# Kernel tuning notes

Hardware: AMD Instinct MI355X
Metric: run time of the kernel (lower is better)

The kernel has to match this reference:

```python
import jax, jax.numpy as jnp
import numpy as np

B, N_PER, E_PER = 100, 1000, 12000  # graphs, nodes/graph, edges/graph
N, E = B * N_PER, B * E_PER
K = int(np.ceil(0.8 * N_PER))  # TopKPooling ratio=0.8 -> 800 kept nodes/graph


def setup_inputs() -> dict:
    key = jax.random.key(0)
    ks = jax.random.split(key, 16)
    g = jnp.repeat(jnp.arange(B, dtype=jnp.int64), E_PER)
    src = g * N_PER + jax.random.randint(ks[0], (E,), 0, N_PER)
    dst = g * N_PER + jax.random.randint(ks[1], (E,), 0, N_PER)
    edge_index = jnp.stack([src, dst]).astype(jnp.int64)
    edge_attr = jax.random.uniform(ks[2], (E,), dtype=jnp.float32) + 0.1  # positive edge weights
    x = jax.random.normal(ks[3], (N, 3), dtype=jnp.float32)
    batch = jnp.repeat(jnp.arange(B, dtype=jnp.int64), N_PER)
    s = 0.1
    return {
        'x': x, 'edge_index': edge_index, 'edge_attr': edge_attr, 'batch': batch,
        'conv1_w': jax.random.normal(ks[4], (3, 64), dtype=jnp.float32) * s,
        'conv1_b': jnp.zeros((64,), dtype=jnp.float32),
        'conv2_w': jax.random.normal(ks[5], (64, 64), dtype=jnp.float32) * s,
        'conv2_b': jnp.zeros((64,), dtype=jnp.float32),
        'pool_w': jax.random.normal(ks[6], (64,), dtype=jnp.float32) * s,
        'lin1_w': jax.random.normal(ks[7], (64, 64), dtype=jnp.float32) * s,
        'lin1_b': jnp.zeros((64,), dtype=jnp.float32),
        'lin2_w': jax.random.normal(ks[8], (64, 32), dtype=jnp.float32) * s,
        'lin2_b': jnp.zeros((32,), dtype=jnp.float32),
        'lin3_w': jax.random.normal(ks[9], (32, 1), dtype=jnp.float32) * s,
        'lin3_b': jnp.zeros((1,), dtype=jnp.float32),
    }


def gcn_conv(x, row, col, ew, W, b):
    # PyG GCNConv with edge_weight and implicit self-loops (weight 1):
    # deg[i] = sum_{e: col=i} ew[e] + 1;  norm_e = d^{-1/2}[row]*ew*d^{-1/2}[col]
    h = x @ W  # [N, out]
    deg = jax.ops.segment_sum(ew, col, num_segments=N) + 1.0
    dinv = jax.lax.rsqrt(deg)
    msg = (dinv[row] * ew * dinv[col])[:, None] * h[row]  # [E, out]
    out = jax.ops.segment_sum(msg, col, num_segments=N)
    out = out + (dinv * dinv)[:, None] * h  # self-loop term
    return out + b


def reference(x, edge_index, edge_attr, batch, conv1_w, conv1_b, conv2_w, conv2_b,
              pool_w, lin1_w, lin1_b, lin2_w, lin2_b, lin3_w, lin3_b):
    row, col = edge_index[0], edge_index[1]
    h = jax.nn.relu(gcn_conv(x, row, col, edge_attr, conv1_w, conv1_b))
    x1 = h.reshape(B, N_PER, 64).mean(axis=1)  # global_mean_pool (equal-size graphs)
    h = jax.nn.relu(gcn_conv(h, row, col, edge_attr, conv2_w, conv2_b))
    # TopKPooling: score = tanh(x.w / ||w||), keep top-K per graph, gate by score
    score = jnp.tanh(h @ pool_w / jnp.linalg.norm(pool_w))  # [N]
    score_bn = score.reshape(B, N_PER)
    vals, idx = jax.lax.top_k(score_bn, K)  # [B, K]
    h_bn = h.reshape(B, N_PER, 64)
    h_sel = jnp.take_along_axis(h_bn, idx[..., None], axis=1) * vals[..., None]
    x2 = h_sel.mean(axis=1)  # global_mean_pool on pooled graph
    z = x1 + x2
    z = jax.nn.relu(z @ lin1_w + lin1_b)
    z = jax.nn.relu(z @ lin2_w + lin2_b)  # dropout is identity in eval mode
    out = jax.nn.sigmoid(z @ lin3_w + lin3_b)[:, 0]
    return out
```

## Files before the change

kernel.cpp:

```cpp
#include <hip/hip_runtime.h>

#define B_G   100
#define N_PER 1000
#define E_PER 12000
#define NTOT  (B_G * N_PER)
#define ETOT  (B_G * E_PER)
#define KSEL  800
#define EPT   12

typedef __attribute__((ext_vector_type(8))) short short8;
typedef __attribute__((ext_vector_type(4))) float float4_;

__device__ __forceinline__ unsigned short f2bf(float f) {
    unsigned u = __float_as_uint(f);
    u += 0x7fffu + ((u >> 16) & 1u);
    return (unsigned short)(u >> 16);
}
__device__ __forceinline__ float bf2f(unsigned short h) {
    return __uint_as_float(((unsigned)h) << 16);
}

__device__ __forceinline__ void load_row_frag(
    const unsigned char* h1s, int src, int kgrp, short8& r0, short8& r1) {
    unsigned a0 = (unsigned)src * 128u + (((unsigned)(kgrp ^ (src & 7))) << 4);
    r0 = *(const short8*)(h1s + a0);
    r1 = *(const short8*)(h1s + (a0 ^ 64u));
}

__global__ __launch_bounds__(1024) void k_all(
    const int* __restrict__ ei, const float* __restrict__ ew,
    const float* __restrict__ x,
    const float* __restrict__ w1, const float* __restrict__ b1,
    const float* __restrict__ w2, const float* __restrict__ b2,
    const float* __restrict__ pw,
    const float* __restrict__ l1w, const float* __restrict__ l1b,
    const float* __restrict__ l2w, const float* __restrict__ l2b,
    const float* __restrict__ l3w, const float* __restrict__ l3b,
    unsigned* __restrict__ csr, float* __restrict__ out) {
    __shared__ __align__(16) unsigned char smem[152832];
    unsigned char* h1s = smem;
    unsigned short* h1u = (unsigned short*)smem;
    int*   ends = (int*)(smem + 128000);
    float* dl   = (float*)(smem + 132096);
    float* x1b  = (float*)(smem + 136192);
    unsigned char* uA = smem + 136448;

    int b = blockIdx.x, tid = threadIdx.x;
    int wid = tid >> 6, lane = tid & 63;
    int gbase = b * N_PER, ebase = b * E_PER;

    int esrc[EPT], edst[EPT]; float eww[EPT];
    int ne = (tid < (E_PER - (EPT - 1) * 1024)) ? EPT : EPT - 1;
#pragma unroll
    for (int i = 0; i < EPT; i++) {
        if (i < ne) {
            int e = tid + i * 1024;
            esrc[i] = ei[ebase + e] - gbase;
            edst[i] = ei[ETOT + ebase + e] - gbase;
            eww[i]  = ew[ebase + e];
        }
    }
    float* wsum = (float*)uA;
    int*   posc = (int*)(uA + 4096);
    ends[tid] = 0;
    wsum[tid] = 0.f;
    __syncthreads();
#pragma unroll
    for (int i = 0; i < EPT; i++)
        if (i < ne) {
            atomicAdd(&ends[edst[i]], 1);
            atomicAdd(&wsum[edst[i]], eww[i]);
        }
    __syncthreads();
    int v = ends[tid];
    int sc = v;
#pragma unroll
    for (int m = 1; m < 64; m <<= 1) {
        int t = __shfl_up(sc, m);
        if (lane >= m) sc += t;
    }
    int* wpart = (int*)x1b;
    if (lane == 63) wpart[wid] = sc;
    __syncthreads();
    if (tid < 16) {
        int s2 = wpart[tid];
#pragma unroll
        for (int m = 1; m < 16; m <<= 1) {
            int t = __shfl_up(s2, m);
            if (tid >= m) s2 += t;
        }
        wpart[tid] = s2;
    }
    __syncthreads();
    int incl = sc + (wid > 0 ? wpart[wid - 1] : 0);
    ends[tid] = incl;
    posc[tid] = incl - v;
    dl[tid] = rsqrtf(wsum[tid] + 1.0f);
    __syncthreads();
#pragma unroll
    for (int i = 0; i < EPT; i++)
        if (i < ne) {
            float cf = dl[esrc[i]] * eww[i] * dl[edst[i]];
            int p = atomicAdd(&posc[edst[i]], 1);
            csr[ebase + p] = ((unsigned)f2bf(cf) << 16) | (unsigned)esrc[i];
        }
    __syncthreads();
    float* aggv = (float*)uA;
    if (tid < N_PER) {
        int s = (tid > 0) ? ends[tid - 1] : 0;
        int e = ends[tid];
        float a0 = 0.f, a1 = 0.f, a2 = 0.f;
        for (int k = s; k < e; k++) {
            unsigned q = csr[ebase + k];
            float cf = __uint_as_float(q & 0xFFFF0000u);
            const float* xs = x + (size_t)(gbase + (int)(q & 0xFFFFu)) * 3;
            a0 += cf * xs[0]; a1 += cf * xs[1]; a2 += cf * xs[2];
        }
        float d2 = dl[tid] * dl[tid];
        const float* xn = x + (size_t)(gbase + tid) * 3;
        aggv[tid * 3 + 0] = a0 + d2 * xn[0];
        aggv[tid * 3 + 1] = a1 + d2 * xn[1];
        aggv[tid * 3 + 2] = a2 + d2 * xn[2];
    }
    __syncthreads();
    {
        float w0 = w1[lane], w1v = w1[64 + lane], w2v = w1[128 + lane], bf = b1[lane];
        float* sred = (float*)(uA + 12288);
        float px = 0.f;
        int swoff = (lane & 7);
        for (int node = wid; node < N_PER; node += 16) {
            float a0 = aggv[node * 3], a1 = aggv[node * 3 + 1], a2 = aggv[node * 3 + 2];
            float h = fmaxf(a0 * w0 + a1 * w1v + a2 * w2v + bf, 0.f);
            h1u[node * 64 + ((((lane >> 3) ^ (node & 7))) << 3) + swoff] = f2bf(h);
            px += h;
        }
        sred[wid * 64 + lane] = px;
        __syncthreads();
        if (tid < 64) {
            float t = 0.f;
            for (int r = 0; r < 16; r++) t += sred[r * 64 + tid];
            x1b[tid] = t * (1.0f / N_PER);
        }
    }
    __syncthreads();
    int kgrp = lane >> 4, nloc = lane & 15;
    short8 AfS[4][2];
#pragma unroll
    for (int ti = 0; ti < 4; ti++) {
        int t = wid + ti * 16;
        if (t >= 63) continue;
        int li = t * 16 + nloc;
        bool valid = li < N_PER;
        float acc[16];
        if (valid) {
            float d2 = dl[li] * dl[li];
            short8 r0, r1;
            load_row_frag(h1s, li, kgrp, r0, r1);
#pragma unroll
            for (int j = 0; j < 8; j++) {
                acc[j]     = d2 * bf2f((unsigned short)r0[j]);
                acc[8 + j] = d2 * bf2f((unsigned short)r1[j]);
            }
        } else {
#pragma unroll
            for (int j = 0; j < 16; j++) acc[j] = 0.f;
        }
        int s = 0, cnt = 0;
        if (valid) {
            s = (li > 0) ? ends[li - 1] : 0;
            cnt = ends[li] - s;
        }
        int mx = cnt;
#pragma unroll
        for (int m = 1; m < 16; m <<= 1) mx = max(mx, __shfl_xor(mx, m));
        int base = ebase + s;
        int cl = max(cnt - 1, 0);
        unsigned q = csr[min(base, ETOT - 1)];
        for (int k = 0; k < mx; k++) {
            unsigned qn = csr[min(base + min(k + 1, cl), ETOT - 1)];
            if (k < cnt) {
                int src = (int)(q & 0xFFFFu);
                float cf = __uint_as_float(q & 0xFFFF0000u);
                short8 r0, r1;
                load_row_frag(h1s, src, kgrp, r0, r1);
#pragma unroll
                for (int j = 0; j < 8; j++) {
                    acc[j]     += cf * bf2f((unsigned short)r0[j]);
                    acc[8 + j] += cf * bf2f((unsigned short)r1[j]);
                }
            }
            q = qn;
        }
        short8 a0, a1;
#pragma unroll
        for (int j = 0; j < 8; j++) {
            a0[j] = (short)f2bf(acc[j]);
            a1[j] = (short)f2bf(acc[8 + j]);
        }
        AfS[ti][0] = a0;
        AfS[ti][1] = a1;
    }
    __syncthreads();
    unsigned long long* keys = (unsigned long long*)uA;
    {
        short8 Bf[2][4];
#pragma unroll
        for (int kh = 0; kh < 2; ++kh)
#pragma unroll
            for (int c = 0; c < 4; ++c) {
                short8 t;
#pragma unroll
                for (int j = 0; j < 8; ++j)
                    t[j] = (short)f2bf(w2[(kh * 32 + kgrp * 8 + j) * 64 + c * 16 + nloc]);
                Bf[kh][c] = t;
            }
        float b2c[4], pwc[4];
#pragma unroll
        for (int c = 0; c < 4; ++c) {
            b2c[c] = b2[c * 16 + nloc];
            pwc[c] = pw[c * 16 + nloc];
        }
        float invn;
        {
            float p = pw[lane], pn = p * p;
#pragma unroll
            for (int m = 32; m; m >>= 1) pn += __shfl_xor(pn, m);
            invn = rsqrtf(pn);
        }
        if (tid >= N_PER) keys[tid] = 0ull;
#pragma unroll
        for (int ti = 0; ti < 4; ti++) {
            int t = wid + ti * 16;
            if (t >= 63) continue;
            float4_ accv[4];
#pragma unroll
            for (int c = 0; c < 4; ++c) accv[c] = (float4_){0.f, 0.f, 0.f, 0.f};
#pragma unroll
            for (int kh = 0; kh < 2; ++kh)
#pragma unroll
                for (int c = 0; c < 4; ++c)
                    accv[c] = __builtin_amdgcn_mfma_f32_16x16x32_bf16(AfS[ti][kh], Bf[kh][c], accv[c], 0, 0, 0);
#pragma unroll
            for (int r2 = 0; r2 < 4; ++r2) {
                int li2 = t * 16 + kgrp * 4 + r2;
                bool valid2 = li2 < N_PER;
                float sp = 0.f;
#pragma unroll
                for (int c = 0; c < 4; ++c) {
                    float hv = fmaxf(accv[c][r2] + b2c[c], 0.f);
                    sp += hv * pwc[c];
                    if (valid2) {
                        int f = c * 16 + nloc;
                        h1u[li2 * 64 + ((((f >> 3) ^ (li2 & 7))) << 3) + (f & 7)] = f2bf(hv);
                    }
                }
#pragma unroll
                for (int m = 1; m < 16; m <<= 1) sp += __shfl_xor(sp, m);
                if (valid2 && nloc == 0) {
                    float scv = tanhf(sp * invn);
                    unsigned bits = __float_as_uint(scv);
                    unsigned u = (bits & 0x80000000u) ? ~bits : (bits | 0x80000000u);
                    keys[li2] = ((unsigned long long)u << 32) | (unsigned)(1023 - li2);
                }
            }
        }
    }
    __syncthreads();
    {
        unsigned long long key = keys[tid];
        for (int k = 2; k <= 1024; k <<= 1) {
            for (int j = k >> 1; j > 0; j >>= 1) {
                bool desc = (tid & k) == 0;
                unsigned long long p;
                if (j >= 64) {
                    keys[tid] = key;
                    __syncthreads();
                    p = keys[tid ^ j];
                    __syncthreads();
                } else {
                    p = __shfl_xor(key, j);
                }
                bool low = (tid & j) == 0;
                bool sw = low ? (desc ? (key < p) : (key > p))
                              : (desc ? (p < key) : (p > key));
                if (sw) key = p;
            }
        }
        keys[tid] = key;
    }
    __syncthreads();
    float* red   = (float*)(uA + 8192);
    float* a1buf = (float*)(uA + 12288);
    float* a2buf = (float*)(uA + 12544);
    float* zbuf  = (float*)(uA + 12672);
    {
        int f = tid & 63, w16 = tid >> 6;
        float acc = 0.f;
        for (int r = w16; r < KSEL; r += 16) {
            unsigned long long key = keys[r];
            int idx = 1023 - (int)(key & 0xFFFFFFFFu);
            unsigned u = (unsigned)(key >> 32);
            unsigned bits = (u & 0x80000000u) ? (u & 0x7FFFFFFFu) : ~u;
            float val = __uint_as_float(bits);
            acc += val * bf2f(h1u[idx * 64 + ((((f >> 3) ^ (idx & 7))) << 3) + (f & 7)]);
        }
        red[tid] = acc;
    }
    __syncthreads();
    if (tid < 64) {
        float s2 = 0.f;
        for (int ww = 0; ww < 16; ww++) s2 += red[ww * 64 + tid];
        zbuf[tid] = x1b[tid] + s2 * (1.0f / KSEL);
    }
    __syncthreads();
    if (tid < 64) {
        float a = l1b[tid];
        for (int k = 0; k < 64; k++) a += zbuf[k] * l1w[k * 64 + tid];
        a1buf[tid] = fmaxf(a, 0.f);
    }
    __syncthreads();
    if (tid < 32) {
        float a = l2b[tid];
        for (int k = 0; k < 64; k++) a += a1buf[k] * l2w[k * 32 + tid];
        a2buf[tid] = fmaxf(a, 0.f);
    }
    __syncthreads();
    if (tid == 0) {
        float t = l3b[0];
        for (int k = 0; k < 32; k++) t += a2buf[k] * l3w[k];
        out[b] = 1.0f / (1.0f + expf(-t));
    }
}

extern "C" void kernel_launch(void* const* d_in, const int* in_sizes, int n_in,
                              void* d_out, int out_size, void* d_ws, size_t ws_size,
                              hipStream_t stream) {
    const float* x   = (const float*)d_in[0];
    const int*   ei  = (const int*)d_in[1];
    const float* ew  = (const float*)d_in[2];
    const float* c1w = (const float*)d_in[4];
    const float* c1b = (const float*)d_in[5];
    const float* c2w = (const float*)d_in[6];
    const float* c2b = (const float*)d_in[7];
    const float* pw  = (const float*)d_in[8];
    const float* l1w = (const float*)d_in[9];
    const float* l1b = (const float*)d_in[10];
    const float* l2w = (const float*)d_in[11];
    const float* l2b = (const float*)d_in[12];
    const float* l3w = (const float*)d_in[13];
    const float* l3b = (const float*)d_in[14];
    float* out = (float*)d_out;
    unsigned* csr = (unsigned*)d_ws;
    (void)ws_size; (void)in_sizes; (void)n_in; (void)out_size;

    k_all<<<B_G, 1024, 0, stream>>>(ei, ew, x, c1w, c1b, c2w, c2b, pw,
                                    l1w, l1b, l2w, l2b, l3w, l3b, csr, out);
}
```

Measured before the change: 191.9 us.

## Split each graph across two blocks and move top-k pooling into second kernel

The fused per-graph kernel becomes two blocks per graph. Each block recomputes degrees and the full layer-1 features but builds CSR and runs the layer-2 MFMA only for its half of the destination nodes. It writes h2, scores and the layer-1 mean to global workspace, and a second kernel does the top-k sort, gated pooling and MLP. Layer-1 aggregation now uses shared-memory atomics on a staged copy of x instead of a CSR gather from global memory. The aim is to fill more of the GPU's compute units (100 blocks to 200). The cost is duplicated per-graph preprocessing, an extra launch, and a global round-trip for h2.

```diff
diff --git a/kernel.cpp b/kernel.cpp
--- a/kernel.cpp
+++ b/kernel.cpp
@@ -7,6 +7,8 @@
 #define ETOT  (B_G * E_PER)
 #define KSEL  800
 #define EPT   12
+#define HALF  512
+#define CSR_CAP 8192
 
 typedef __attribute__((ext_vector_type(8))) short short8;
 typedef __attribute__((ext_vector_type(4))) float float4_;
@@ -27,27 +29,32 @@
     r1 = *(const short8*)(h1s + (a0 ^ 64u));
 }
 
-__global__ __launch_bounds__(1024) void k_all(
+__global__ __launch_bounds__(1024) void k_main(
     const int* __restrict__ ei, const float* __restrict__ ew,
     const float* __restrict__ x,
     const float* __restrict__ w1, const float* __restrict__ b1,
     const float* __restrict__ w2, const float* __restrict__ b2,
     const float* __restrict__ pw,
-    const float* __restrict__ l1w, const float* __restrict__ l1b,
-    const float* __restrict__ l2w, const float* __restrict__ l2b,
-    const float* __restrict__ l3w, const float* __restrict__ l3b,
-    unsigned* __restrict__ csr, float* __restrict__ out) {
-    __shared__ __align__(16) unsigned char smem[152832];
+    unsigned* __restrict__ csr, unsigned short* __restrict__ h2g,
+    float* __restrict__ scoreg, float* __restrict__ x1g) {
+    __shared__ __align__(16) unsigned char smem[160768];
     unsigned char* h1s = smem;
     unsigned short* h1u = (unsigned short*)smem;
     int*   ends = (int*)(smem + 128000);
     float* dl   = (float*)(smem + 132096);
-    float* x1b  = (float*)(smem + 136192);
-    unsigned char* uA = smem + 136448;
-
-    int b = blockIdx.x, tid = threadIdx.x;
-    int wid = tid >> 6, lane = tid & 63;
-    int gbase = b * N_PER, ebase = b * E_PER;
+    float* xl   = (float*)(smem + 136192);
+    float* sred = (float*)(smem + 136192);
+    unsigned char* U = smem + 148480;
+    int*   posc  = (int*)U;
+    float* wsum  = (float*)(U + 4096);
+    int*   wpart = (int*)(U + 8192);
+    float* aggv  = (float*)U;
+
+    int blk = blockIdx.x;
+    int g = blk >> 1, h = blk & 1;
+    int tid = threadIdx.x, wid = tid >> 6, lane = tid & 63;
+    int gbase = g * N_PER, ebase = g * E_PER;
+    unsigned* csrg = csr + (size_t)blk * CSR_CAP;
 
     int esrc[EPT], edst[EPT]; float eww[EPT];
     int ne = (tid < (E_PER - (EPT - 1) * 1024)) ? EPT : EPT - 1;
@@ -60,16 +67,15 @@
             eww[i]  = ew[ebase + e];
         }
     }
-    float* wsum = (float*)uA;
-    int*   posc = (int*)(uA + 4096);
     ends[tid] = 0;
     wsum[tid] = 0.f;
+    for (int i = tid; i < N_PER * 3; i += 1024) xl[i] = x[(size_t)gbase * 3 + i];
     __syncthreads();
 #pragma unroll
     for (int i = 0; i < EPT; i++)
         if (i < ne) {
-            atomicAdd(&ends[edst[i]], 1);
             atomicAdd(&wsum[edst[i]], eww[i]);
+            if ((edst[i] >> 9) == h) atomicAdd(&ends[edst[i]], 1);
         }
     __syncthreads();
     int v = ends[tid];
@@ -79,7 +85,6 @@
         int t = __shfl_up(sc, m);
         if (lane >= m) sc += t;
     }
-    int* wpart = (int*)x1b;
     if (lane == 63) wpart[wid] = sc;
     __syncthreads();
     if (tid < 16) {
@@ -99,57 +104,51 @@
     __syncthreads();
 #pragma unroll
     for (int i = 0; i < EPT; i++)
+        if (i < ne && (edst[i] >> 9) == h) {
+            float cf = dl[esrc[i]] * eww[i] * dl[edst[i]];
+            int p = atomicAdd(&posc[edst[i]], 1);
+            csrg[p] = ((unsigned)f2bf(cf) << 16) | (unsigned)esrc[i];
+        }
+    __syncthreads();
+    for (int i = tid; i < N_PER; i += 1024) {
+        float d2 = dl[i] * dl[i];
+        aggv[i * 3 + 0] = d2 * xl[i * 3 + 0];
+        aggv[i * 3 + 1] = d2 * xl[i * 3 + 1];
+        aggv[i * 3 + 2] = d2 * xl[i * 3 + 2];
+    }
+    __syncthreads();
+#pragma unroll
+    for (int i = 0; i < EPT; i++)
         if (i < ne) {
             float cf = dl[esrc[i]] * eww[i] * dl[edst[i]];
-            int p = atomicAdd(&posc[edst[i]], 1);
-            csr[ebase + p] = ((unsigned)f2bf(cf) << 16) | (unsigned)esrc[i];
-        }
-    __syncthreads();
-    float* aggv = (float*)uA;
-    if (tid < N_PER) {
-        int s = (tid > 0) ? ends[tid - 1] : 0;
-        int e = ends[tid];
-        float a0 = 0.f, a1 = 0.f, a2 = 0.f;
-        for (int k = s; k < e; k++) {
-            unsigned q = csr[ebase + k];
-            float cf = __uint_as_float(q & 0xFFFF0000u);
-            const float* xs = x + (size_t)(gbase + (int)(q & 0xFFFFu)) * 3;
-            a0 += cf * xs[0]; a1 += cf * xs[1]; a2 += cf * xs[2];
-        }
-        float d2 = dl[tid] * dl[tid];
-        const float* xn = x + (size_t)(gbase + tid) * 3;
-        aggv[tid * 3 + 0] = a0 + d2 * xn[0];
-        aggv[tid * 3 + 1] = a1 + d2 * xn[1];
-        aggv[tid * 3 + 2] = a2 + d2 * xn[2];
-    }
+            atomicAdd(&aggv[edst[i] * 3 + 0], cf * xl[esrc[i] * 3 + 0]);
+            atomicAdd(&aggv[edst[i] * 3 + 1], cf * xl[esrc[i] * 3 + 1]);
+            atomicAdd(&aggv[edst[i] * 3 + 2], cf * xl[esrc[i] * 3 + 2]);
+        }
     __syncthreads();
     {
         float w0 = w1[lane], w1v = w1[64 + lane], w2v = w1[128 + lane], bf = b1[lane];
-        float* sred = (float*)(uA + 12288);
         float px = 0.f;
-        int swoff = (lane & 7);
         for (int node = wid; node < N_PER; node += 16) {
             float a0 = aggv[node * 3], a1 = aggv[node * 3 + 1], a2 = aggv[node * 3 + 2];
-            float h = fmaxf(a0 * w0 + a1 * w1v + a2 * w2v + bf, 0.f);
-            h1u[node * 64 + ((((lane >> 3) ^ (node & 7))) << 3) + swoff] = f2bf(h);
-            px += h;
+            float hv = fmaxf(a0 * w0 + a1 * w1v + a2 * w2v + bf, 0.f);
+            h1u[node * 64 + ((((lane >> 3) ^ (node & 7))) << 3) + (lane & 7)] = f2bf(hv);
+            px += hv;
         }
         sred[wid * 64 + lane] = px;
-        __syncthreads();
-        if (tid < 64) {
-            float t = 0.f;
-            for (int r = 0; r < 16; r++) t += sred[r * 64 + tid];
-            x1b[tid] = t * (1.0f / N_PER);
-        }
-    }
-    __syncthreads();
+    }
+    __syncthreads();
+    if (h == 0 && tid < 64) {
+        float t = 0.f;
+        for (int r = 0; r < 16; r++) t += sred[r * 64 + tid];
+        x1g[g * 64 + tid] = t * (1.0f / N_PER);
+    }
     int kgrp = lane >> 4, nloc = lane & 15;
-    short8 AfS[4][2];
-#pragma unroll
-    for (int ti = 0; ti < 4; ti++) {
+    short8 AfS[2][2];
+#pragma unroll
+    for (int ti = 0; ti < 2; ti++) {
         int t = wid + ti * 16;
-        if (t >= 63) continue;
-        int li = t * 16 + nloc;
+        int li = h * HALF + t * 16 + nloc;
         bool valid = li < N_PER;
         float acc[16];
         if (valid) {
@@ -173,11 +172,10 @@
         int mx = cnt;
 #pragma unroll
         for (int m = 1; m < 16; m <<= 1) mx = max(mx, __shfl_xor(mx, m));
-        int base = ebase + s;
         int cl = max(cnt - 1, 0);
-        unsigned q = csr[min(base, ETOT - 1)];
+        unsigned q = csrg[min(s, CSR_CAP - 1)];
         for (int k = 0; k < mx; k++) {
-            unsigned qn = csr[min(base + min(k + 1, cl), ETOT - 1)];
+            unsigned qn = csrg[min(s + min(k + 1, cl), CSR_CAP - 1)];
             if (k < cnt) {
                 int src = (int)(q & 0xFFFFu);
                 float cf = __uint_as_float(q & 0xFFFF0000u);
@@ -200,8 +198,6 @@
         AfS[ti][0] = a0;
         AfS[ti][1] = a1;
     }
-    __syncthreads();
-    unsigned long long* keys = (unsigned long long*)uA;
     {
         short8 Bf[2][4];
 #pragma unroll
@@ -227,11 +223,9 @@
             for (int m = 32; m; m >>= 1) pn += __shfl_xor(pn, m);
             invn = rsqrtf(pn);
         }
-        if (tid >= N_PER) keys[tid] = 0ull;
-#pragma unroll
-        for (int ti = 0; ti < 4; ti++) {
+#pragma unroll
+        for (int ti = 0; ti < 2; ti++) {
             int t = wid + ti * 16;
-            if (t >= 63) continue;
             float4_ accv[4];
 #pragma unroll
             for (int c = 0; c < 4; ++c) accv[c] = (float4_){0.f, 0.f, 0.f, 0.f};
@@ -242,28 +236,41 @@
                     accv[c] = __builtin_amdgcn_mfma_f32_16x16x32_bf16(AfS[ti][kh], Bf[kh][c], accv[c], 0, 0, 0);
 #pragma unroll
             for (int r2 = 0; r2 < 4; ++r2) {
-                int li2 = t * 16 + kgrp * 4 + r2;
+                int li2 = h * HALF + t * 16 + kgrp * 4 + r2;
                 bool valid2 = li2 < N_PER;
                 float sp = 0.f;
 #pragma unroll
                 for (int c = 0; c < 4; ++c) {
                     float hv = fmaxf(accv[c][r2] + b2c[c], 0.f);
                     sp += hv * pwc[c];
-                    if (valid2) {
-                        int f = c * 16 + nloc;
-                        h1u[li2 * 64 + ((((f >> 3) ^ (li2 & 7))) << 3) + (f & 7)] = f2bf(hv);
-                    }
+                    if (valid2) h2g[(size_t)(gbase + li2) * 64 + c * 16 + nloc] = f2bf(hv);
                 }
 #pragma unroll
                 for (int m = 1; m < 16; m <<= 1) sp += __shfl_xor(sp, m);
-                if (valid2 && nloc == 0) {
-                    float scv = tanhf(sp * invn);
-                    unsigned bits = __float_as_uint(scv);
-                    unsigned u = (bits & 0x80000000u) ? ~bits : (bits | 0x80000000u);
-                    keys[li2] = ((unsigned long long)u << 32) | (unsigned)(1023 - li2);
-                }
-            }
-        }
+                if (valid2 && nloc == 0) scoreg[gbase + li2] = tanhf(sp * invn);
+            }
+        }
+    }
+}
+
+__global__ __launch_bounds__(1024) void k_post(
+    const float* __restrict__ scoreg, const unsigned short* __restrict__ h2g,
+    const float* __restrict__ x1g,
+    const float* __restrict__ l1w, const float* __restrict__ l1b,
+    const float* __restrict__ l2w, const float* __restrict__ l2b,
+    const float* __restrict__ l3w, const float* __restrict__ l3b,
+    float* __restrict__ out) {
+    __shared__ unsigned long long keys[1024];
+    __shared__ float red[1024];
+    __shared__ float zbuf[64], a1buf[64], a2buf[32];
+    int b = blockIdx.x, tid = threadIdx.x;
+    if (tid < N_PER) {
+        float sc = scoreg[b * N_PER + tid];
+        unsigned bits = __float_as_uint(sc);
+        unsigned u = (bits & 0x80000000u) ? ~bits : (bits | 0x80000000u);
+        keys[tid] = ((unsigned long long)u << 32) | (unsigned)(1023 - tid);
+    } else {
+        keys[tid] = 0ull;
     }
     __syncthreads();
     {
@@ -289,10 +296,6 @@
         keys[tid] = key;
     }
     __syncthreads();
-    float* red   = (float*)(uA + 8192);
-    float* a1buf = (float*)(uA + 12288);
-    float* a2buf = (float*)(uA + 12544);
-    float* zbuf  = (float*)(uA + 12672);
     {
         int f = tid & 63, w16 = tid >> 6;
         float acc = 0.f;
@@ -302,7 +305,7 @@
             unsigned u = (unsigned)(key >> 32);
             unsigned bits = (u & 0x80000000u) ? (u & 0x7FFFFFFFu) : ~u;
             float val = __uint_as_float(bits);
-            acc += val * bf2f(h1u[idx * 64 + ((((f >> 3) ^ (idx & 7))) << 3) + (f & 7)]);
+            acc += val * bf2f(h2g[(size_t)(b * N_PER + idx) * 64 + f]);
         }
         red[tid] = acc;
     }
@@ -310,7 +313,7 @@
     if (tid < 64) {
         float s2 = 0.f;
         for (int ww = 0; ww < 16; ww++) s2 += red[ww * 64 + tid];
-        zbuf[tid] = x1b[tid] + s2 * (1.0f / KSEL);
+        zbuf[tid] = x1g[b * 64 + tid] + s2 * (1.0f / KSEL);
     }
     __syncthreads();
     if (tid < 64) {
@@ -350,9 +353,18 @@
     const float* l3w = (const float*)d_in[13];
     const float* l3b = (const float*)d_in[14];
     float* out = (float*)d_out;
-    unsigned* csr = (unsigned*)d_ws;
+
+    char* ws = (char*)d_ws;
+    size_t o = 0;
+    auto alloc = [&](size_t bytes) { size_t cur = o; o += (bytes + 511) & ~(size_t)511; return cur; };
+    unsigned*       csr    = (unsigned*)(ws + alloc((size_t)B_G * 2 * CSR_CAP * 4));
+    unsigned short* h2g    = (unsigned short*)(ws + alloc((size_t)NTOT * 64 * 2));
+    float*          scoreg = (float*)(ws + alloc((size_t)NTOT * 4));
+    float*          x1g    = (float*)(ws + alloc((size_t)B_G * 64 * 4));
     (void)ws_size; (void)in_sizes; (void)n_in; (void)out_size;
 
-    k_all<<<B_G, 1024, 0, stream>>>(ei, ew, x, c1w, c1b, c2w, c2b, pw,
-                                    l1w, l1b, l2w, l2b, l3w, l3b, csr, out);
-}
+    k_main<<<B_G * 2, 1024, 0, stream>>>(ei, ew, x, c1w, c1b, c2w, c2b, pw,
+                                         csr, h2g, scoreg, x1g);
+    k_post<<<B_G, 1024, 0, stream>>>(scoreg, h2g, x1g,
+                                     l1w, l1b, l2w, l2b, l3w, l3b, out);
+}
```

After: 228.9 us. 1.19x slower.

## Stage x in LDS, scatter layer-1 aggregation with atomics, interleave layer-2 gathers

Applied to the files above, without the earlier changes.

The first-layer aggregation now copies the graph's x into shared memory and accumulates edge messages with shared-memory atomicAdd while the CSR is built. This removes the separate CSR walk over global x and one barrier. The layer-2 gather loop is restructured so the four node tiles per wave advance together, each with its own prefetched CSR entry, which exposes more independent loads per iteration. The cost is more registers (4x16 accumulators), float atomic contention on 3000 LDS addresses, nondeterministic summation order, and the removal of the t>=63 skip, so out-of-range tiles now do extra work.

```diff
diff --git a/kernel.cpp b/kernel.cpp
--- a/kernel.cpp
+++ b/kernel.cpp
@@ -40,10 +40,15 @@
     __shared__ __align__(16) unsigned char smem[152832];
     unsigned char* h1s = smem;
     unsigned short* h1u = (unsigned short*)smem;
+    float* xl   = (float*)smem;
+    float* wsum = (float*)(smem + 12032);
     int*   ends = (int*)(smem + 128000);
     float* dl   = (float*)(smem + 132096);
-    float* x1b  = (float*)(smem + 136192);
+    int*   wpart = (int*)(smem + 136192);
+    float* x1b   = (float*)(smem + 136192);
     unsigned char* uA = smem + 136448;
+    float* aggv = (float*)uA;
+    int*   posc = (int*)(uA + 12288);
 
     int b = blockIdx.x, tid = threadIdx.x;
     int wid = tid >> 6, lane = tid & 63;
@@ -60,8 +65,10 @@
             eww[i]  = ew[ebase + e];
         }
     }
-    float* wsum = (float*)uA;
-    int*   posc = (int*)(uA + 4096);
+    for (int i = tid; i < N_PER * 3; i += 1024) {
+        xl[i] = x[(size_t)gbase * 3 + i];
+        aggv[i] = 0.f;
+    }
     ends[tid] = 0;
     wsum[tid] = 0.f;
     __syncthreads();
@@ -79,7 +86,6 @@
         int t = __shfl_up(sc, m);
         if (lane >= m) sc += t;
     }
-    int* wpart = (int*)x1b;
     if (lane == 63) wpart[wid] = sc;
     __syncthreads();
     if (tid < 16) {
@@ -97,43 +103,34 @@
     posc[tid] = incl - v;
     dl[tid] = rsqrtf(wsum[tid] + 1.0f);
     __syncthreads();
+    if (tid < N_PER) {
+        float d2 = dl[tid] * dl[tid];
+        atomicAdd(&aggv[tid * 3 + 0], d2 * xl[tid * 3 + 0]);
+        atomicAdd(&aggv[tid * 3 + 1], d2 * xl[tid * 3 + 1]);
+        atomicAdd(&aggv[tid * 3 + 2], d2 * xl[tid * 3 + 2]);
+    }
 #pragma unroll
     for (int i = 0; i < EPT; i++)
         if (i < ne) {
             float cf = dl[esrc[i]] * eww[i] * dl[edst[i]];
             int p = atomicAdd(&posc[edst[i]], 1);
             csr[ebase + p] = ((unsigned)f2bf(cf) << 16) | (unsigned)esrc[i];
-        }
-    __syncthreads();
-    float* aggv = (float*)uA;
-    if (tid < N_PER) {
-        int s = (tid > 0) ? ends[tid - 1] : 0;
-        int e = ends[tid];
-        float a0 = 0.f, a1 = 0.f, a2 = 0.f;
-        for (int k = s; k < e; k++) {
-            unsigned q = csr[ebase + k];
-            float cf = __uint_as_float(q & 0xFFFF0000u);
-            const float* xs = x + (size_t)(gbase + (int)(q & 0xFFFFu)) * 3;
-            a0 += cf * xs[0]; a1 += cf * xs[1]; a2 += cf * xs[2];
-        }
-        float d2 = dl[tid] * dl[tid];
-        const float* xn = x + (size_t)(gbase + tid) * 3;
-        aggv[tid * 3 + 0] = a0 + d2 * xn[0];
-        aggv[tid * 3 + 1] = a1 + d2 * xn[1];
-        aggv[tid * 3 + 2] = a2 + d2 * xn[2];
-    }
+            atomicAdd(&aggv[edst[i] * 3 + 0], cf * xl[esrc[i] * 3 + 0]);
+            atomicAdd(&aggv[edst[i] * 3 + 1], cf * xl[esrc[i] * 3 + 1]);
+            atomicAdd(&aggv[edst[i] * 3 + 2], cf * xl[esrc[i] * 3 + 2]);
+        }
     __syncthreads();
     {
         float w0 = w1[lane], w1v = w1[64 + lane], w2v = w1[128 + lane], bf = b1[lane];
         float* sred = (float*)(uA + 12288);
         float px = 0.f;
-        int swoff = (lane & 7);
         for (int node = wid; node < N_PER; node += 16) {
             float a0 = aggv[node * 3], a1 = aggv[node * 3 + 1], a2 = aggv[node * 3 + 2];
-            float h = fmaxf(a0 * w0 + a1 * w1v + a2 * w2v + bf, 0.f);
-            h1u[node * 64 + ((((lane >> 3) ^ (node & 7))) << 3) + swoff] = f2bf(h);
-            px += h;
-        }
+            float hv = fmaxf(a0 * w0 + a1 * w1v + a2 * w2v + bf, 0.f);
+            h1u[node * 64 + ((((lane >> 3) ^ (node & 7))) << 3) + (lane & 7)] = f2bf(hv);
+            px += hv;
+        }
+        __syncthreads();
         sred[wid * 64 + lane] = px;
         __syncthreads();
         if (tid < 64) {
@@ -142,28 +139,28 @@
             x1b[tid] = t * (1.0f / N_PER);
         }
     }
-    __syncthreads();
     int kgrp = lane >> 4, nloc = lane & 15;
-    short8 AfS[4][2];
+    float acc[4][16];
+    int sA[4], cntA[4], mxA[4];
+    unsigned pre[4];
+    int kmax = 0;
 #pragma unroll
     for (int ti = 0; ti < 4; ti++) {
         int t = wid + ti * 16;
-        if (t >= 63) continue;
         int li = t * 16 + nloc;
         bool valid = li < N_PER;
-        float acc[16];
         if (valid) {
             float d2 = dl[li] * dl[li];
             short8 r0, r1;
             load_row_frag(h1s, li, kgrp, r0, r1);
 #pragma unroll
             for (int j = 0; j < 8; j++) {
-                acc[j]     = d2 * bf2f((unsigned short)r0[j]);
-                acc[8 + j] = d2 * bf2f((unsigned short)r1[j]);
+                acc[ti][j]     = d2 * bf2f((unsigned short)r0[j]);
+                acc[ti][8 + j] = d2 * bf2f((unsigned short)r1[j]);
             }
         } else {
 #pragma unroll
-            for (int j = 0; j < 16; j++) acc[j] = 0.f;
+            for (int j = 0; j < 16; j++) acc[ti][j] = 0.f;
         }
         int s = 0, cnt = 0;
         if (valid) {
@@ -173,29 +170,39 @@
         int mx = cnt;
 #pragma unroll
         for (int m = 1; m < 16; m <<= 1) mx = max(mx, __shfl_xor(mx, m));
-        int base = ebase + s;
-        int cl = max(cnt - 1, 0);
-        unsigned q = csr[min(base, ETOT - 1)];
-        for (int k = 0; k < mx; k++) {
-            unsigned qn = csr[min(base + min(k + 1, cl), ETOT - 1)];
-            if (k < cnt) {
-                int src = (int)(q & 0xFFFFu);
-                float cf = __uint_as_float(q & 0xFFFF0000u);
-                short8 r0, r1;
-                load_row_frag(h1s, src, kgrp, r0, r1);
-#pragma unroll
-                for (int j = 0; j < 8; j++) {
-                    acc[j]     += cf * bf2f((unsigned short)r0[j]);
-                    acc[8 + j] += cf * bf2f((unsigned short)r1[j]);
+        sA[ti] = s; cntA[ti] = cnt; mxA[ti] = mx;
+        kmax = max(kmax, mx);
+        pre[ti] = csr[min(ebase + s, ETOT - 1)];
+    }
+    for (int k = 0; k < kmax; k++) {
+#pragma unroll
+        for (int ti = 0; ti < 4; ti++) {
+            if (k < mxA[ti]) {
+                unsigned q = pre[ti];
+                int nxt = sA[ti] + min(k + 1, max(cntA[ti] - 1, 0));
+                pre[ti] = csr[min(ebase + nxt, ETOT - 1)];
+                if (k < cntA[ti]) {
+                    int src = (int)(q & 0xFFFFu);
+                    float cf = __uint_as_float(q & 0xFFFF0000u);
+                    short8 r0, r1;
+                    load_row_frag(h1s, src, kgrp, r0, r1);
+#pragma unroll
+                    for (int j = 0; j < 8; j++) {
+                        acc[ti][j]     += cf * bf2f((unsigned short)r0[j]);
+                        acc[ti][8 + j] += cf * bf2f((unsigned short)r1[j]);
+                    }
                 }
             }
-            q = qn;
-        }
+        }
+    }
+    short8 AfS[4][2];
+#pragma unroll
+    for (int ti = 0; ti < 4; ti++) {
         short8 a0, a1;
 #pragma unroll
         for (int j = 0; j < 8; j++) {
-            a0[j] = (short)f2bf(acc[j]);
-            a1[j] = (short)f2bf(acc[8 + j]);
+            a0[j] = (short)f2bf(acc[ti][j]);
+            a1[j] = (short)f2bf(acc[ti][8 + j]);
         }
         AfS[ti][0] = a0;
         AfS[ti][1] = a1;
@@ -295,16 +302,16 @@
     float* zbuf  = (float*)(uA + 12672);
     {
         int f = tid & 63, w16 = tid >> 6;
-        float acc = 0.f;
+        float acc2 = 0.f;
         for (int r = w16; r < KSEL; r += 16) {
             unsigned long long key = keys[r];
             int idx = 1023 - (int)(key & 0xFFFFFFFFu);
             unsigned u = (unsigned)(key >> 32);
             unsigned bits = (u & 0x80000000u) ? (u & 0x7FFFFFFFu) : ~u;
             float val = __uint_as_float(bits);
-            acc += val * bf2f(h1u[idx * 64 + ((((f >> 3) ^ (idx & 7))) << 3) + (f & 7)]);
-        }
-        red[tid] = acc;
+            acc2 += val * bf2f(h1u[idx * 64 + ((((f >> 3) ^ (idx & 7))) << 3) + (f & 7)]);
+        }
+        red[tid] = acc2;
     }
     __syncthreads();
     if (tid < 64) {
```

New measurement: 235.4 us. 22.7% more time.

## Store node features as custom 8-bit floats and keep CSR in LDS

Applied to the files above, without the earlier changes.

Node features for both conv layers are now stored in LDS as a custom 7-bit exponent/mantissa code (a biased fp32 truncation, sign dropped since values are post-ReLU) instead of bf16. This halves the per-edge gather bytes and frees LDS, which now also holds the CSR and x, so they no longer go through global memory. The degree computation is reworked: raw edge weights go into the CSR, the normalization is folded into prescaled source features, and the destination scale is applied once after aggregation. This risks accuracy loss from the 3-bit mantissa format, and it drops a prefetch pipeline and a barrier.

```diff
diff --git a/kernel.cpp b/kernel.cpp
--- a/kernel.cpp
+++ b/kernel.cpp
@@ -16,15 +16,16 @@
     u += 0x7fffu + ((u >> 16) & 1u);
     return (unsigned short)(u >> 16);
 }
-__device__ __forceinline__ float bf2f(unsigned short h) {
-    return __uint_as_float(((unsigned)h) << 16);
-}
-
-__device__ __forceinline__ void load_row_frag(
-    const unsigned char* h1s, int src, int kgrp, short8& r0, short8& r1) {
-    unsigned a0 = (unsigned)src * 128u + (((unsigned)(kgrp ^ (src & 7))) << 4);
-    r0 = *(const short8*)(h1s + a0);
-    r1 = *(const short8*)(h1s + (a0 ^ 64u));
+__device__ __forceinline__ float upk(unsigned q) {
+    return __uint_as_float(q & 0xFFFF0000u);
+}
+__device__ __forceinline__ float dec_raw(unsigned byte7f) {
+    return __uint_as_float(byte7f << 20);
+}
+__device__ __forceinline__ unsigned enc_fp8(float z) {
+    unsigned u = __float_as_uint(z * 0x1p-120f);
+    u += 0x7FFFFu + ((u >> 20) & 1u);
+    return u >> 20;
 }
 
 __global__ __launch_bounds__(1024) void k_all(
@@ -36,14 +37,18 @@
     const float* __restrict__ l1w, const float* __restrict__ l1b,
     const float* __restrict__ l2w, const float* __restrict__ l2b,
     const float* __restrict__ l3w, const float* __restrict__ l3b,
-    unsigned* __restrict__ csr, float* __restrict__ out) {
-    __shared__ __align__(16) unsigned char smem[152832];
-    unsigned char* h1s = smem;
-    unsigned short* h1u = (unsigned short*)smem;
-    int*   ends = (int*)(smem + 128000);
-    float* dl   = (float*)(smem + 132096);
-    float* x1b  = (float*)(smem + 136192);
-    unsigned char* uA = smem + 136448;
+    float* __restrict__ out) {
+    __shared__ __align__(16) unsigned char smem[136832];
+    unsigned char* zs = smem;
+    float* xl = (float*)smem;
+    unsigned* csr = (unsigned*)(smem + 64000);
+    int*   ends = (int*)(smem + 112000);
+    float* dl   = (float*)(smem + 116096);
+    int*   posc = (int*)(smem + 116096);
+    int*   wpart = (int*)(smem + 120192);
+    float* x1b   = (float*)(smem + 120192);
+    unsigned char* uA = smem + 120448;
+    float* aggv = (float*)uA;
 
     int b = blockIdx.x, tid = threadIdx.x;
     int wid = tid >> 6, lane = tid & 63;
@@ -60,17 +65,12 @@
             eww[i]  = ew[ebase + e];
         }
     }
-    float* wsum = (float*)uA;
-    int*   posc = (int*)(uA + 4096);
     ends[tid] = 0;
-    wsum[tid] = 0.f;
+    for (int i = tid; i < N_PER * 3; i += 1024) xl[i] = x[(size_t)gbase * 3 + i];
     __syncthreads();
 #pragma unroll
     for (int i = 0; i < EPT; i++)
-        if (i < ne) {
-            atomicAdd(&ends[edst[i]], 1);
-            atomicAdd(&wsum[edst[i]], eww[i]);
-        }
+        if (i < ne) atomicAdd(&ends[edst[i]], 1);
     __syncthreads();
     int v = ends[tid];
     int sc = v;
@@ -79,7 +79,6 @@
         int t = __shfl_up(sc, m);
         if (lane >= m) sc += t;
     }
-    int* wpart = (int*)x1b;
     if (lane == 63) wpart[wid] = sc;
     __syncthreads();
     if (tid < 16) {
@@ -95,44 +94,62 @@
     int incl = sc + (wid > 0 ? wpart[wid - 1] : 0);
     ends[tid] = incl;
     posc[tid] = incl - v;
-    dl[tid] = rsqrtf(wsum[tid] + 1.0f);
     __syncthreads();
 #pragma unroll
     for (int i = 0; i < EPT; i++)
         if (i < ne) {
-            float cf = dl[esrc[i]] * eww[i] * dl[edst[i]];
             int p = atomicAdd(&posc[edst[i]], 1);
-            csr[ebase + p] = ((unsigned)f2bf(cf) << 16) | (unsigned)esrc[i];
-        }
-    __syncthreads();
-    float* aggv = (float*)uA;
+            csr[p] = ((unsigned)f2bf(eww[i]) << 16) | (unsigned)esrc[i];
+        }
+    __syncthreads();
+    float dmy = 0.f;
+    int s0i = 0, e0i = 0;
     if (tid < N_PER) {
-        int s = (tid > 0) ? ends[tid - 1] : 0;
-        int e = ends[tid];
-        float a0 = 0.f, a1 = 0.f, a2 = 0.f;
-        for (int k = s; k < e; k++) {
-            unsigned q = csr[ebase + k];
-            float cf = __uint_as_float(q & 0xFFFF0000u);
-            const float* xs = x + (size_t)(gbase + (int)(q & 0xFFFFu)) * 3;
-            a0 += cf * xs[0]; a1 += cf * xs[1]; a2 += cf * xs[2];
-        }
-        float d2 = dl[tid] * dl[tid];
-        const float* xn = x + (size_t)(gbase + tid) * 3;
-        aggv[tid * 3 + 0] = a0 + d2 * xn[0];
-        aggv[tid * 3 + 1] = a1 + d2 * xn[1];
-        aggv[tid * 3 + 2] = a2 + d2 * xn[2];
+        s0i = tid ? ends[tid - 1] : 0;
+        e0i = ends[tid];
+        float s0 = 0.f, s1 = 0.f;
+        int k = s0i;
+        for (; k + 2 <= e0i; k += 2) { s0 += upk(csr[k]); s1 += upk(csr[k + 1]); }
+        if (k < e0i) s0 += upk(csr[k]);
+        dmy = rsqrtf(s0 + s1 + 1.0f);
+        dl[tid] = dmy;
+        xl[tid * 3 + 0] *= dmy;
+        xl[tid * 3 + 1] *= dmy;
+        xl[tid * 3 + 2] *= dmy;
+    }
+    __syncthreads();
+    if (tid < N_PER) {
+        float a0 = xl[tid * 3 + 0], a1 = xl[tid * 3 + 1], a2 = xl[tid * 3 + 2];
+        for (int k = s0i; k < e0i; k++) {
+            unsigned q = csr[k];
+            int i0 = (int)(q & 0xFFFFu) * 3;
+            float wv = upk(q);
+            a0 += wv * xl[i0]; a1 += wv * xl[i0 + 1]; a2 += wv * xl[i0 + 2];
+        }
+        aggv[tid * 3 + 0] = dmy * a0;
+        aggv[tid * 3 + 1] = dmy * a1;
+        aggv[tid * 3 + 2] = dmy * a2;
     }
     __syncthreads();
     {
         float w0 = w1[lane], w1v = w1[64 + lane], w2v = w1[128 + lane], bf = b1[lane];
         float* sred = (float*)(uA + 12288);
         float px = 0.f;
-        int swoff = (lane & 7);
+        int chunk = (lane & 31) >> 3;
+        int word  = ((lane >= 32) ? 2 : 0) + ((lane & 7) >> 2);
         for (int node = wid; node < N_PER; node += 16) {
             float a0 = aggv[node * 3], a1 = aggv[node * 3 + 1], a2 = aggv[node * 3 + 2];
-            float h = fmaxf(a0 * w0 + a1 * w1v + a2 * w2v + bf, 0.f);
-            h1u[node * 64 + ((((lane >> 3) ^ (node & 7))) << 3) + swoff] = f2bf(h);
-            px += h;
+            float hv = fmaxf(a0 * w0 + a1 * w1v + a2 * w2v + bf, 0.f);
+            px += hv;
+            unsigned byte = enc_fp8(dl[node] * hv);
+            unsigned t1 = __shfl_xor(byte, 1);
+            unsigned v16 = (lane & 1) ? (t1 | (byte << 8)) : (byte | (t1 << 8));
+            unsigned t2 = __shfl_xor(v16, 2);
+            unsigned v32 = (lane & 2) ? (t2 | (v16 << 16)) : (v16 | (t2 << 16));
+            if ((lane & 3) == 0) {
+                int cs = chunk ^ ((node >> 1) & 3);
+                *(unsigned*)(zs + node * 64 + cs * 16 + word * 4) = v32;
+            }
         }
         sred[wid * 64 + lane] = px;
         __syncthreads();
@@ -142,60 +159,54 @@
             x1b[tid] = t * (1.0f / N_PER);
         }
     }
-    __syncthreads();
     int kgrp = lane >> 4, nloc = lane & 15;
     short8 AfS[4][2];
 #pragma unroll
     for (int ti = 0; ti < 4; ti++) {
         int t = wid + ti * 16;
-        if (t >= 63) continue;
         int li = t * 16 + nloc;
         bool valid = li < N_PER;
         float acc[16];
+        int s = 0, cn = 0;
         if (valid) {
-            float d2 = dl[li] * dl[li];
-            short8 r0, r1;
-            load_row_frag(h1s, li, kgrp, r0, r1);
-#pragma unroll
-            for (int j = 0; j < 8; j++) {
-                acc[j]     = d2 * bf2f((unsigned short)r0[j]);
-                acc[8 + j] = d2 * bf2f((unsigned short)r1[j]);
-            }
+            uint4 rv = *(const uint4*)(zs + li * 64 + ((kgrp ^ ((li >> 1) & 3)) << 4));
+#pragma unroll
+            for (int j = 0; j < 4; j++) {
+                acc[j]      = dec_raw((rv.x >> (8 * j)) & 0x7Fu);
+                acc[4 + j]  = dec_raw((rv.y >> (8 * j)) & 0x7Fu);
+                acc[8 + j]  = dec_raw((rv.z >> (8 * j)) & 0x7Fu);
+                acc[12 + j] = dec_raw((rv.w >> (8 * j)) & 0x7Fu);
+            }
+            s = li ? ends[li - 1] : 0;
+            cn = ends[li] - s;
         } else {
 #pragma unroll
             for (int j = 0; j < 16; j++) acc[j] = 0.f;
         }
-        int s = 0, cnt = 0;
-        if (valid) {
-            s = (li > 0) ? ends[li - 1] : 0;
-            cnt = ends[li] - s;
-        }
-        int mx = cnt;
+        int mx = cn;
 #pragma unroll
         for (int m = 1; m < 16; m <<= 1) mx = max(mx, __shfl_xor(mx, m));
-        int base = ebase + s;
-        int cl = max(cnt - 1, 0);
-        unsigned q = csr[min(base, ETOT - 1)];
         for (int k = 0; k < mx; k++) {
-            unsigned qn = csr[min(base + min(k + 1, cl), ETOT - 1)];
-            if (k < cnt) {
+            if (k < cn) {
+                unsigned q = csr[s + k];
                 int src = (int)(q & 0xFFFFu);
-                float cf = __uint_as_float(q & 0xFFFF0000u);
-                short8 r0, r1;
-                load_row_frag(h1s, src, kgrp, r0, r1);
-#pragma unroll
-                for (int j = 0; j < 8; j++) {
-                    acc[j]     += cf * bf2f((unsigned short)r0[j]);
-                    acc[8 + j] += cf * bf2f((unsigned short)r1[j]);
+                float wv = upk(q);
+                uint4 rv = *(const uint4*)(zs + src * 64 + ((kgrp ^ ((src >> 1) & 3)) << 4));
+#pragma unroll
+                for (int j = 0; j < 4; j++) {
+                    acc[j]      += wv * dec_raw((rv.x >> (8 * j)) & 0x7Fu);
+                    acc[4 + j]  += wv * dec_raw((rv.y >> (8 * j)) & 0x7Fu);
+                    acc[8 + j]  += wv * dec_raw((rv.z >> (8 * j)) & 0x7Fu);
+                    acc[12 + j] += wv * dec_raw((rv.w >> (8 * j)) & 0x7Fu);
                 }
             }
-            q = qn;
-        }
+        }
+        float scale = (valid ? dl[li] : 0.f) * 0x1p120f;
         short8 a0, a1;
 #pragma unroll
         for (int j = 0; j < 8; j++) {
-            a0[j] = (short)f2bf(acc[j]);
-            a1[j] = (short)f2bf(acc[8 + j]);
+            a0[j] = (short)f2bf(scale * acc[j]);
+            a1[j] = (short)f2bf(scale * acc[8 + j]);
         }
         AfS[ti][0] = a0;
         AfS[ti][1] = a1;
@@ -249,10 +260,7 @@
                 for (int c = 0; c < 4; ++c) {
                     float hv = fmaxf(accv[c][r2] + b2c[c], 0.f);
                     sp += hv * pwc[c];
-                    if (valid2) {
-                        int f = c * 16 + nloc;
-                        h1u[li2 * 64 + ((((f >> 3) ^ (li2 & 7))) << 3) + (f & 7)] = f2bf(hv);
-                    }
+                    if (valid2) zs[li2 * 64 + c * 16 + nloc] = (unsigned char)enc_fp8(hv);
                 }
 #pragma unroll
                 for (int m = 1; m < 16; m <<= 1) sp += __shfl_xor(sp, m);
@@ -295,16 +303,16 @@
     float* zbuf  = (float*)(uA + 12672);
     {
         int f = tid & 63, w16 = tid >> 6;
-        float acc = 0.f;
+        float acc2 = 0.f;
         for (int r = w16; r < KSEL; r += 16) {
             unsigned long long key = keys[r];
             int idx = 1023 - (int)(key & 0xFFFFFFFFu);
             unsigned u = (unsigned)(key >> 32);
             unsigned bits = (u & 0x80000000u) ? (u & 0x7FFFFFFFu) : ~u;
-            float val = __uint_as_float(bits);
-            acc += val * bf2f(h1u[idx * 64 + ((((f >> 3) ^ (idx & 7))) << 3) + (f & 7)]);
-        }
-        red[tid] = acc;
+            float valS = __uint_as_float(bits) * 0x1p120f;
+            acc2 += valS * dec_raw((unsigned)zs[idx * 64 + f] & 0x7Fu);
+        }
+        red[tid] = acc2;
     }
     __syncthreads();
     if (tid < 64) {
@@ -350,9 +358,8 @@
     const float* l3w = (const float*)d_in[13];
     const float* l3b = (const float*)d_in[14];
     float* out = (float*)d_out;
-    unsigned* csr = (unsigned*)d_ws;
-    (void)ws_size; (void)in_sizes; (void)n_in; (void)out_size;
+    (void)d_ws; (void)ws_size; (void)in_sizes; (void)n_in; (void)out_size;
 
     k_all<<<B_G, 1024, 0, stream>>>(ei, ew, x, c1w, c1b, c2w, c2b, pw,
-                                    l1w, l1b, l2w, l2b, l3w, l3b, csr, out);
-}
+                                    l1w, l1b, l2w, l2b, l3w, l3b, out);
+}
```

Measured after the change: 181.0 us. 5.7% less time.
